# Kernel optimization log

Hardware: AMD Instinct MI355X
Metric: run time of the kernel (lower is better)

## Reference

```python
import jax, jax.numpy as jnp
import numpy as np

B, T, D, H = 512, 128, 256, 512  # batch, seq_len, input_dim, hidden_dim
L = T  # dense output size == seq_len


def setup_inputs() -> dict:
    key = jax.random.key(0)
    ks = jax.random.split(key, 12)
    s = 0.05
    return {
        "inputs": jax.random.normal(ks[0], (B, T, D), jnp.float32),
        "target_indices": jax.random.randint(ks[1], (B, T), 0, T),
        "enc_Wih": jax.random.normal(ks[2], (4 * H, D), jnp.float32) * s,
        "enc_Whh": jax.random.normal(ks[3], (4 * H, H), jnp.float32) * s,
        "enc_bih": jnp.zeros((4 * H,), jnp.float32),
        "enc_bhh": jnp.zeros((4 * H,), jnp.float32),
        "dec_Wih": jax.random.normal(ks[4], (4 * H, D), jnp.float32) * s,
        "dec_Whh": jax.random.normal(ks[5], (4 * H, H), jnp.float32) * s,
        "dec_bih": jnp.zeros((4 * H,), jnp.float32),
        "dec_bhh": jnp.zeros((4 * H,), jnp.float32),
        "Wd": jax.random.normal(ks[6], (L, H), jnp.float32) * s,
        "bd": jnp.zeros((L,), jnp.float32),
        "Wr": jax.random.normal(ks[7], (4, H), jnp.float32) * (2.0 / np.sqrt(H)),
        "br": jnp.zeros((4,), jnp.float32),
    }


def _lstm_cell(x, h, c, Wih, Whh, bih, bhh):
    gates = x @ Wih.T + h @ Whh.T + bih + bhh
    i, f, g, o = jnp.split(gates, 4, axis=-1)  # torch gate order i,f,g,o
    c = jax.nn.sigmoid(f) * c + jax.nn.sigmoid(i) * jnp.tanh(g)
    h = jax.nn.sigmoid(o) * jnp.tanh(c)
    return h, c


def reference(inputs, target_indices, enc_Wih, enc_Whh, enc_bih, enc_bhh,
              dec_Wih, dec_Whh, dec_bih, dec_bhh, Wd, bd, Wr, br):
    b, t, d = inputs.shape
    hdim = enc_Whh.shape[1]

    # Encoder LSTM over time (identical every step in the original -> compute once)
    def enc_step(carry, x_t):
        h, c = carry
        h, c = _lstm_cell(x_t, h, c, enc_Wih, enc_Whh, enc_bih, enc_bhh)
        return (h, c), h

    h0 = jnp.zeros((b, hdim), inputs.dtype)
    _, enc_hs = jax.lax.scan(enc_step, (h0, h0), inputs.transpose(1, 0, 2))
    enc = enc_hs.transpose(1, 0, 2)  # [B, T, H]

    batch_ar = jnp.arange(b)

    def dec_step(carry, idx_t):
        h, c, mask, x = carry
        h, c = _lstm_cell(x, h, c, dec_Wih, dec_Whh, dec_bih, dec_bhh)
        scores = jnp.einsum('bh,bth->bt', h, enc)
        attn = jax.nn.softmax(scores, axis=-1)
        ctx = jnp.einsum('bt,bth->bh', attn, enc)
        logits = ctx @ Wd.T + bd                       # [B, L]
        logits = jnp.where(mask > 0, -jnp.inf, logits)  # mask previously selected
        rot = ctx @ Wr.T + br                          # [B, 4]
        idx = jnp.clip(idx_t, 0, t - 1)
        mask = jnp.maximum(mask, jax.nn.one_hot(idx, mask.shape[1], dtype=mask.dtype))
        x_next = inputs[batch_ar, idx]
        return (h, c, mask, x_next), (logits, rot)

    mask0 = jnp.zeros((b, Wd.shape[0]), inputs.dtype)
    x0 = jnp.zeros((b, d), inputs.dtype)
    _, (all_logits, all_rot) = jax.lax.scan(
        dec_step, (h0, h0, mask0, x0), target_indices.T)
    return all_logits.transpose(1, 0, 2), all_rot.transpose(1, 0, 2)
```

## Files before the change

kernel.cpp:

```cpp
#include <hip/hip_runtime.h>
#include <hip/hip_bf16.h>
#include <hip/hip_fp16.h>
#include <math.h>

#define B_ 512
#define T_ 128
#define D_ 256
#define H_ 512
#define L_ 128

#define NEG_BIG (-1e30f)

typedef __hip_bfloat16 bf16;
typedef _Float16 f16x8 __attribute__((ext_vector_type(8)));
typedef float f32x4 __attribute__((ext_vector_type(4)));

__device__ __forceinline__ f32x4 mfma16(f16x8 a, f16x8 b, f32x4 c) {
  return __builtin_amdgcn_mfma_f32_16x16x32_f16(a, b, c, 0, 0, 0);
}

__device__ __forceinline__ float sigm(float x) { return 1.0f / (1.0f + expf(-x)); }

__device__ __forceinline__ float bf2f_bits(unsigned short u) {
  unsigned int i = ((unsigned int)u) << 16;
  float f; __builtin_memcpy(&f, &i, 4);
  return f;
}
__device__ __forceinline__ unsigned short f2bf_bits(float f) {
  unsigned int i; __builtin_memcpy(&i, &f, 4);
  unsigned int r = i + 0x7FFFu + ((i >> 16) & 1u);
  return (unsigned short)(r >> 16);
}

template <int F32>
__device__ __forceinline__ float ld1t(const void* base, size_t idx) {
  if (F32) return ((const float*)base)[idx];
  unsigned short u; __builtin_memcpy(&u, (const bf16*)base + idx, 2);
  return bf2f_bits(u);
}
template <int F32>
__device__ __forceinline__ void load8t(const void* base, size_t idx, float* d) {
  if (F32) {
    float4 x = *(const float4*)((const float*)base + idx);
    float4 y = *(const float4*)((const float*)base + idx + 4);
    d[0] = x.x; d[1] = x.y; d[2] = x.z; d[3] = x.w;
    d[4] = y.x; d[5] = y.y; d[6] = y.z; d[7] = y.w;
  } else {
    union { float4 f4; unsigned short u[8]; } q;
    q.f4 = *(const float4*)((const bf16*)base + idx);
#pragma unroll
    for (int i = 0; i < 8; ++i) d[i] = bf2f_bits(q.u[i]);
  }
}
template <int F32>
__device__ __forceinline__ void st1t(void* base, size_t idx, float v) {
  if (F32) ((float*)base)[idx] = v;
  else {
    unsigned short u = f2bf_bits(v);
    __builtin_memcpy((bf16*)base + idx, &u, 2);
  }
}

__global__ void probe_kernel(const void* x, int* flag) {
  __shared__ int cnt;
  if (threadIdx.x == 0) cnt = 0;
  __syncthreads();
  const unsigned short* u = (const unsigned short*)x;
  int wild = 0;
  for (int i = threadIdx.x; i < 16384; i += 256) {
    float v = bf2f_bits(u[2 * i]);
    float av = fabsf(v);
    if (!(av <= 1024.0f) || (v != 0.0f && av < 1e-20f)) wild++;
  }
  atomicAdd(&cnt, wild);
  __syncthreads();
  if (threadIdx.x == 0) flag[0] = (cnt > 512) ? 1 : 0;
}

__global__ void zero_kernel(float* __restrict__ p, int n4) {
  int i = blockIdx.x * blockDim.x + threadIdx.x;
  if (i < n4) ((float4*)p)[i] = make_float4(0.f, 0.f, 0.f, 0.f);
}

__global__ void first_sel_kernel(const int* __restrict__ tidx, int* __restrict__ fs) {
  __shared__ int row[L_];
  __shared__ int idxs[T_];
  int b = blockIdx.x;
  row[threadIdx.x] = 1 << 30;
  int v = tidx[b * T_ + threadIdx.x];
  idxs[threadIdx.x] = min(max(v, 0), T_ - 1);
  __syncthreads();
  if (threadIdx.x == 0) {
    for (int s = 0; s < T_; ++s) {
      int idx = idxs[s];
      if (row[idx] > s) row[idx] = s;
    }
  }
  __syncthreads();
  fs[b * L_ + threadIdx.x] = row[threadIdx.x];
}

template <int F32>
__device__ void pack_w_body(const void* Wih, const void* Whh, const void* bih,
                            const void* bhh, __half* Wpk, float* bs) {
  int np = blockIdx.x;
  int g = np & 3, j = np >> 2;
  int worig = g * H_ + j;
  for (int k = threadIdx.x; k < D_ + H_; k += 256) {
    float v = (k < D_) ? ld1t<F32>(Wih, (size_t)worig * D_ + k)
                       : ld1t<F32>(Whh, (size_t)worig * H_ + (k - D_));
    Wpk[(size_t)np * (D_ + H_) + k] = __float2half(v);
  }
  if (threadIdx.x == 0)
    bs[np] = ld1t<F32>(bih, worig) + ld1t<F32>(bhh, worig);
}
__global__ __launch_bounds__(256) void pack_w(const void* Wih, const void* Whh,
    const void* bih, const void* bhh, __half* Wpk, float* bs, const int* flagp) {
  if (*flagp) pack_w_body<1>(Wih, Whh, bih, bhh, Wpk, bs);
  else        pack_w_body<0>(Wih, Whh, bih, bhh, Wpk, bs);
}

template <int F32>
__device__ void pack16_body(const void* src, __half* dst, int n8) {
  int i = blockIdx.x * blockDim.x + threadIdx.x;
  if (i >= n8) return;
  float w[8];
  load8t<F32>(src, (size_t)i * 8, w);
  union { float4 f4; __half h[8]; } u;
#pragma unroll
  for (int q = 0; q < 8; ++q) u.h[q] = __float2half(w[q]);
  *(float4*)(dst + (size_t)i * 8) = u.f4;
}
__global__ __launch_bounds__(256) void pack16(const void* src, __half* dst, int n8,
                                              const int* flagp) {
  if (*flagp) pack16_body<1>(src, dst, n8);
  else        pack16_body<0>(src, dst, n8);
}

__global__ __launch_bounds__(256) void gather_x(const __half* __restrict__ X16,
                                                const int* __restrict__ tidx,
                                                __half* __restrict__ Xdec) {
  const int row = blockIdx.x * 8 + (threadIdx.x >> 5);
  const int c8 = (threadIdx.x & 31) * 8;
  const int b = row >> 7;
  const int s = row & (T_ - 1);
  float4 v;
  if (s == 0) {
    v = make_float4(0.f, 0.f, 0.f, 0.f);
  } else {
    int tsel = min(max(tidx[b * T_ + s - 1], 0), T_ - 1);
    v = *(const float4*)(X16 + ((size_t)b * T_ + tsel) * D_ + c8);
  }
  *(float4*)(Xdec + (size_t)row * D_ + c8) = v;
}

__global__ __launch_bounds__(256) void transpose_enc(const __half* __restrict__ enc,
                                                     __half* __restrict__ encT) {
  __shared__ __half tile[32][33];
  const int b = blockIdx.x;
  const int t0 = blockIdx.y * 32;
  const int h0 = blockIdx.z * 32;
  const int c = threadIdx.x & 31;
  const int r = threadIdx.x >> 5;
#pragma unroll
  for (int rr = 0; rr < 32; rr += 8)
    tile[rr + r][c] = enc[((size_t)b * T_ + t0 + rr + r) * H_ + h0 + c];
  __syncthreads();
#pragma unroll
  for (int rr = 0; rr < 32; rr += 8)
    encT[((size_t)b * H_ + h0 + rr + r) * T_ + t0 + c] = tile[c][rr + r];
}

__device__ __forceinline__ void cell_epi(const f32x4& acc, const float4& bias,
                                         float& c, unsigned short* hdst,
                                         int bb, int t, int jj) {
  float gi = acc[0] + bias.x;
  float gf = acc[1] + bias.y;
  float gg = acc[2] + bias.z;
  float go = acc[3] + bias.w;
  c = sigm(gf) * c + sigm(gi) * tanhf(gg);
  float hh = sigm(go) * tanhf(c);
  unsigned short hu = __half_as_ushort(__float2half(hh));
  __hip_atomic_store(hdst + ((size_t)bb * T_ + t) * H_ + jj, hu,
                     __ATOMIC_RELAXED, __HIP_MEMORY_SCOPE_AGENT);
}

__global__ __launch_bounds__(256, 2) void lstm_persist(
    const __half* __restrict__ Xenc, const __half* __restrict__ Xdec,
    const __half* __restrict__ WpkE, const float* __restrict__ bsE,
    const __half* __restrict__ WpkD, const float* __restrict__ bsD,
    __half* __restrict__ enc, __half* __restrict__ hdec, int* __restrict__ bar) {
  const int tid = threadIdx.x;
  const int lane = tid & 63;
  const int w = tid >> 6;
  const int r15 = lane & 15;
  const int g4 = lane >> 4;
  const int m0 = blockIdx.x * 64 + (w >> 1) * 32;
  const int b0 = blockIdx.y * 64 + (w & 1) * 32;
  const int bb0 = b0 + r15;
  const int bb1 = bb0 + 16;
  const int p = blockIdx.z;
  int* flags = bar + (p * 8 + blockIdx.y) * 64;
  const int fl = lane & 31;
  const f32x4 z4 = {0.f, 0.f, 0.f, 0.f};

  const __half* Wpk = p ? WpkD : WpkE;
  const float* bs = p ? bsD : bsE;
  const __half* Xp = p ? Xdec : Xenc;
  __half* hbuf = p ? hdec : enc;
  unsigned short* hw = (unsigned short*)hbuf;
  const __half* hb = hbuf;
  const __half* aXp0 = Wpk + (size_t)(m0 + r15) * (D_ + H_) + g4 * 8;
  const __half* aXp1 = aXp0 + (size_t)16 * (D_ + H_);
  f16x8 aH0[16], aH1[16];
#pragma unroll
  for (int ks = 0; ks < 16; ++ks) {
    aH0[ks] = *(const f16x8*)(aXp0 + D_ + ks * 32);
    aH1[ks] = *(const f16x8*)(aXp1 + D_ + ks * 32);
  }
  const int nb0 = m0 + g4 * 4;
  const float4 bias0 = *(const float4*)(bs + nb0);
  const float4 bias1 = *(const float4*)(bs + nb0 + 16);
  const int j0 = nb0 >> 2;
  const int j1 = j0 + 4;
  float c00 = 0.f, c01 = 0.f, c10 = 0.f, c11 = 0.f;

  for (int t = 0; t < T_; ++t) {
    f32x4 acc00 = z4, acc01 = z4, acc10 = z4, acc11 = z4;
    {
      const __half* x0p = Xp + ((size_t)bb0 * T_ + t) * D_ + g4 * 8;
      const __half* x1p = Xp + ((size_t)bb1 * T_ + t) * D_ + g4 * 8;
#pragma unroll
      for (int ks = 0; ks < 8; ++ks) {
        f16x8 a0 = *(const f16x8*)(aXp0 + ks * 32);
        f16x8 a1 = *(const f16x8*)(aXp1 + ks * 32);
        f16x8 bx0 = *(const f16x8*)(x0p + ks * 32);
        f16x8 bx1 = *(const f16x8*)(x1p + ks * 32);
        acc00 = mfma16(a0, bx0, acc00);
        acc01 = mfma16(a0, bx1, acc01);
        acc10 = mfma16(a1, bx0, acc10);
        acc11 = mfma16(a1, bx1, acc11);
      }
    }
    if (t) {
      int v = __hip_atomic_load(flags + fl, __ATOMIC_RELAXED,
                                __HIP_MEMORY_SCOPE_AGENT);
      while (!__all(v >= t)) {
        __builtin_amdgcn_s_sleep(1);
        v = __hip_atomic_load(flags + fl, __ATOMIC_RELAXED,
                              __HIP_MEMORY_SCOPE_AGENT);
      }
      const __half* h0p = hb + ((size_t)bb0 * T_ + (t - 1)) * H_ + g4 * 8;
      const __half* h1p = hb + ((size_t)bb1 * T_ + (t - 1)) * H_ + g4 * 8;
      asm volatile("" : "+v"(h0p), "+v"(h1p));
#pragma unroll
      for (int ks = 0; ks < 16; ++ks) {
        f16x8 bh0 = *(const f16x8*)(h0p + ks * 32);
        f16x8 bh1 = *(const f16x8*)(h1p + ks * 32);
        acc00 = mfma16(aH0[ks], bh0, acc00);
        acc01 = mfma16(aH0[ks], bh1, acc01);
        acc10 = mfma16(aH1[ks], bh0, acc10);
        acc11 = mfma16(aH1[ks], bh1, acc11);
      }
    }
    cell_epi(acc00, bias0, c00, hw, bb0, t, j0);
    cell_epi(acc01, bias0, c01, hw, bb1, t, j0);
    cell_epi(acc10, bias1, c10, hw, bb0, t, j1);
    cell_epi(acc11, bias1, c11, hw, bb1, t, j1);
    if (t + 1 < T_) {
      __syncthreads();
      if (tid == 0)
        __hip_atomic_store(flags + blockIdx.x, t + 1, __ATOMIC_RELAXED,
                           __HIP_MEMORY_SCOPE_AGENT);
    }
  }
}

template <int F32>
__device__ void attend_body(const __half* __restrict__ hdec, const __half* __restrict__ enc,
                            const __half* __restrict__ encT, const __half* __restrict__ Wd16,
                            const void* __restrict__ bd, const void* __restrict__ Wr,
                            const void* __restrict__ br, const int* __restrict__ fs,
                            void* __restrict__ out) {
  __shared__ __align__(16) __half Plds[4][16 * 128];
  __shared__ __align__(16) __half Clds[4][16 * 128];
  const int b = blockIdx.x;
  const int sbase = blockIdx.y * 64;
  const int tid = threadIdx.x;
  const int lane = tid & 63;
  const int w = tid >> 6;
  const int r15 = lane & 15;
  const int g4 = lane >> 4;
  const int sw = sbase + w * 16;
  const __half* encb = enc + (size_t)b * T_ * H_;
  const f32x4 z4 = {0.f, 0.f, 0.f, 0.f};
  f32x4 sacc[8];
#pragma unroll
  for (int i = 0; i < 8; ++i) sacc[i] = z4;
  {
    const __half* hdp = hdec + ((size_t)b * T_ + (sw + r15)) * H_ + g4 * 8;
    for (int k0 = 0; k0 < H_; k0 += 32) {
      f16x8 bv = *(const f16x8*)(hdp + k0);
      const __half* ap = encb + (size_t)r15 * H_ + g4 * 8 + k0;
#pragma unroll
      for (int ms = 0; ms < 8; ++ms)
        sacc[ms] = mfma16(*(const f16x8*)(ap + (size_t)ms * 16 * H_), bv, sacc[ms]);
    }
  }
  float mx = -INFINITY;
#pragma unroll
  for (int ms = 0; ms < 8; ++ms)
#pragma unroll
    for (int q = 0; q < 4; ++q) mx = fmaxf(mx, sacc[ms][q]);
  mx = fmaxf(mx, __shfl_xor(mx, 16));
  mx = fmaxf(mx, __shfl_xor(mx, 32));
  float sum = 0.f;
  float pv[32];
#pragma unroll
  for (int ms = 0; ms < 8; ++ms)
#pragma unroll
    for (int q = 0; q < 4; ++q) {
      float e = expf(sacc[ms][q] - mx);
      pv[ms * 4 + q] = e;
      sum += e;
    }
  sum += __shfl_xor(sum, 16);
  sum += __shfl_xor(sum, 32);
  const float inv = 1.0f / sum;
  {
    char* pw = (char*)Plds[w];
    const int swz = (r15 & 7) << 4;
#pragma unroll
    for (int ms = 0; ms < 8; ++ms)
#pragma unroll
      for (int q = 0; q < 4; ++q) {
        int t = ms * 16 + g4 * 4 + q;
        *(__half*)(pw + r15 * 256 + ((t * 2) ^ swz)) = __float2half(pv[ms * 4 + q] * inv);
      }
  }
  __syncthreads();
  f32x4 lacc[8];
#pragma unroll
  for (int i = 0; i < 8; ++i) lacc[i] = z4;
  float racc = 0.f;
  const int sl4 = lane >> 2;
  const int rr4 = lane & 3;
  const char* pr = (const char*)Plds[w];
  char* cw = (char*)Clds[w];
  const char* cr = (const char*)Clds[w];
  const int aswz = (r15 & 7) << 4;
  for (int hc = 0; hc < 4; ++hc) {
    f32x4 cacc[8];
#pragma unroll
    for (int i = 0; i < 8; ++i) cacc[i] = z4;
#pragma unroll
    for (int k0 = 0; k0 < T_; k0 += 32) {
      f16x8 av = *(const f16x8*)(pr + r15 * 256 + (((k0 + g4 * 8) * 2) ^ aswz));
      const __half* bp = encT + ((size_t)b * H_ + hc * 128 + r15) * T_ + g4 * 8 + k0;
#pragma unroll
      for (int ns = 0; ns < 8; ++ns)
        cacc[ns] = mfma16(av, *(const f16x8*)(bp + (size_t)ns * 16 * T_), cacc[ns]);
    }
    __syncthreads();
#pragma unroll
    for (int ns = 0; ns < 8; ++ns)
#pragma unroll
      for (int q = 0; q < 4; ++q) {
        int s = g4 * 4 + q;
        int h2 = (ns * 16 + r15) * 2;
        *(__half*)(cw + s * 256 + (h2 ^ ((s & 7) << 4))) = __float2half(cacc[ns][q]);
      }
    __syncthreads();
#pragma unroll
    for (int kk = 0; kk < 128; kk += 32) {
      f16x8 av = *(const f16x8*)(cr + r15 * 256 + (((kk + g4 * 8) * 2) ^ aswz));
      const __half* wp = Wd16 + (size_t)r15 * H_ + hc * 128 + kk + g4 * 8;
#pragma unroll
      for (int nl = 0; nl < 8; ++nl)
        lacc[nl] = mfma16(av, *(const f16x8*)(wp + (size_t)nl * 16 * H_), lacc[nl]);
    }
    {
      const int rswz = (sl4 & 7) << 4;
#pragma unroll
      for (int g = 0; g < 16; ++g) {
        union { float4 f4; __half h[8]; } u;
        u.f4 = *(const float4*)(cr + sl4 * 256 + ((g * 16) ^ rswz));
#pragma unroll
        for (int q = 0; q < 8; ++q)
          racc += __half2float(u.h[q]) *
                  ld1t<F32>(Wr, (size_t)rr4 * H_ + hc * 128 + g * 8 + q);
      }
    }
  }
#pragma unroll
  for (int nl = 0; nl < 8; ++nl)
#pragma unroll
    for (int q = 0; q < 4; ++q) {
      int sg = sw + g4 * 4 + q;
      int l = nl * 16 + r15;
      float v = lacc[nl][q] + ld1t<F32>(bd, l);
      if (fs[b * L_ + l] < sg) v = NEG_BIG;
      st1t<F32>(out, ((size_t)b * T_ + sg) * L_ + l, v);
    }
  {
    float v = racc + ld1t<F32>(br, rr4);
    st1t<F32>(out, (size_t)B_ * T_ * L_ + ((size_t)b * T_ + (sw + sl4)) * 4 + rr4, v);
  }
}

__global__ __launch_bounds__(256) void attend_mfma(
    const __half* hdec, const __half* enc, const __half* encT, const __half* Wd16,
    const void* bd, const void* Wr, const void* br, const int* fs, void* out,
    const int* flagp) {
  if (*flagp) attend_body<1>(hdec, enc, encT, Wd16, bd, Wr, br, fs, out);
  else        attend_body<0>(hdec, enc, encT, Wd16, bd, Wr, br, fs, out);
}

static inline size_t al256(size_t x) { return (x + 255) & ~(size_t)255; }

extern "C" void kernel_launch(void* const* d_in, const int* in_sizes, int n_in,
                              void* d_out, int out_size, void* d_ws, size_t ws_size,
                              hipStream_t stream) {
  const void* inputs = d_in[0];
  const int* tidx = (const int*)d_in[1];
  const void* eWih = d_in[2];
  const void* eWhh = d_in[3];
  const void* eBih = d_in[4];
  const void* eBhh = d_in[5];
  const void* dWih = d_in[6];
  const void* dWhh = d_in[7];
  const void* dBih = d_in[8];
  const void* dBhh = d_in[9];
  const void* Wd = d_in[10];
  const void* bd = d_in[11];
  const void* Wr = d_in[12];
  const void* br = d_in[13];

  char* pp = (char*)d_ws;
  int* flag = (int*)pp;        pp += 256;
  int* fs = (int*)pp;          pp += al256((size_t)B_ * L_ * 4);
  __half* WpkE = (__half*)pp;  pp += (size_t)4 * H_ * (D_ + H_) * 2;
  __half* WpkD = (__half*)pp;  pp += (size_t)4 * H_ * (D_ + H_) * 2;
  float* bsE = (float*)pp;     pp += (size_t)4 * H_ * 4;
  float* bsD = (float*)pp;     pp += (size_t)4 * H_ * 4;
  __half* Wd16 = (__half*)pp;  pp += (size_t)L_ * H_ * 2;
  __half* X16 = (__half*)pp;   pp += (size_t)B_ * T_ * D_ * 2;
  __half* enc = (__half*)pp;   pp += (size_t)B_ * T_ * H_ * 2;
  __half* encT = (__half*)pp;  pp += (size_t)B_ * H_ * T_ * 2;
  __half* hdec = (__half*)pp;  pp += (size_t)B_ * T_ * H_ * 2;
  int* bar = (int*)pp;         pp += 4096;
  __half* Xdec = encT;

  probe_kernel<<<1, 256, 0, stream>>>(inputs, flag);
  pack_w<<<4 * H_, 256, 0, stream>>>(eWih, eWhh, eBih, eBhh, WpkE, bsE, flag);
  pack_w<<<4 * H_, 256, 0, stream>>>(dWih, dWhh, dBih, dBhh, WpkD, bsD, flag);
  pack16<<<(B_ * T_ * D_ / 8 + 255) / 256, 256, 0, stream>>>(
      inputs, X16, B_ * T_ * D_ / 8, flag);
  pack16<<<(L_ * H_ / 8 + 255) / 256, 256, 0, stream>>>(Wd, Wd16, L_ * H_ / 8, flag);
  first_sel_kernel<<<B_, 128, 0, stream>>>(tidx, fs);
  gather_x<<<B_ * T_ / 8, 256, 0, stream>>>(X16, tidx, Xdec);
  zero_kernel<<<1, 256, 0, stream>>>((float*)bar, 256);

  lstm_persist<<<dim3(32, 8, 2), 256, 0, stream>>>(X16, Xdec, WpkE, bsE, WpkD, bsD,
                                                   enc, hdec, bar);

  transpose_enc<<<dim3(B_, T_ / 32, H_ / 32), 256, 0, stream>>>(enc, encT);

  attend_mfma<<<dim3(B_, 2), 256, 0, stream>>>(hdec, enc, encT, Wd16, bd, Wr, br,
                                               fs, d_out, flag);
}
```

Before: 2.098 ms.

## Place LSTM sync groups on a single XCD and stage h through LDS

Re-maps the persistent LSTM grid so that each group of 16 workgroups sharing a batch slice and its flag barrier is scheduled on one XCD, using the round-robin workgroup-to-XCD assignment. It checks HW_REG_XCC_ID at runtime and uses plain stores when the whole group is co-located, falling back to agent-scope atomics otherwise. Tiles grow to 128 gate rows × 32 batch per workgroup. The hidden state is staged through swizzled LDS so each thread writes one coalesced 8-byte chunk instead of scattered 2-byte atomics. The goal is cheaper cross-workgroup communication and fewer global stores. The cost is an extra __syncthreads, a startup handshake, and a dependence on the dispatch-order assumption.

```diff
diff --git a/kernel.cpp b/kernel.cpp
--- a/kernel.cpp
+++ b/kernel.cpp
@@ -171,45 +171,37 @@
     encT[((size_t)b * H_ + h0 + rr + r) * T_ + t0 + c] = tile[c][rr + r];
 }
 
-__device__ __forceinline__ void cell_epi(const f32x4& acc, const float4& bias,
-                                         float& c, unsigned short* hdst,
-                                         int bb, int t, int jj) {
+#define SWZ(b, j) ((j) ^ (((b) & 7) << 2))
+
+__device__ __forceinline__ void cell_f(const f32x4& acc, const float4& bias,
+                                       float& c, float* hh) {
   float gi = acc[0] + bias.x;
   float gf = acc[1] + bias.y;
   float gg = acc[2] + bias.z;
   float go = acc[3] + bias.w;
   c = sigm(gf) * c + sigm(gi) * tanhf(gg);
-  float hh = sigm(go) * tanhf(c);
-  unsigned short hu = __half_as_ushort(__float2half(hh));
-  __hip_atomic_store(hdst + ((size_t)bb * T_ + t) * H_ + jj, hu,
-                     __ATOMIC_RELAXED, __HIP_MEMORY_SCOPE_AGENT);
-}
-
-__global__ __launch_bounds__(256, 2) void lstm_persist(
-    const __half* __restrict__ Xenc, const __half* __restrict__ Xdec,
-    const __half* __restrict__ WpkE, const float* __restrict__ bsE,
-    const __half* __restrict__ WpkD, const float* __restrict__ bsD,
-    __half* __restrict__ enc, __half* __restrict__ hdec, int* __restrict__ bar) {
+  *hh = sigm(go) * tanhf(c);
+}
+
+template <int FAST>
+__device__ void lstm_chain(const __half* __restrict__ Xp,
+                           const __half* __restrict__ Wpk,
+                           const float* __restrict__ bs,
+                           __half* __restrict__ hbuf,
+                           int tile, int bg, int* __restrict__ flags) {
+  __shared__ __half hstage[32][32];
   const int tid = threadIdx.x;
   const int lane = tid & 63;
   const int w = tid >> 6;
   const int r15 = lane & 15;
   const int g4 = lane >> 4;
-  const int m0 = blockIdx.x * 64 + (w >> 1) * 32;
-  const int b0 = blockIdx.y * 64 + (w & 1) * 32;
+  const int m0 = tile * 128 + w * 32;
+  const int b0 = bg * 32;
   const int bb0 = b0 + r15;
   const int bb1 = bb0 + 16;
-  const int p = blockIdx.z;
-  int* flags = bar + (p * 8 + blockIdx.y) * 64;
-  const int fl = lane & 31;
+  const int fl = lane & 15;
   const f32x4 z4 = {0.f, 0.f, 0.f, 0.f};
 
-  const __half* Wpk = p ? WpkD : WpkE;
-  const float* bs = p ? bsD : bsE;
-  const __half* Xp = p ? Xdec : Xenc;
-  __half* hbuf = p ? hdec : enc;
-  unsigned short* hw = (unsigned short*)hbuf;
-  const __half* hb = hbuf;
   const __half* aXp0 = Wpk + (size_t)(m0 + r15) * (D_ + H_) + g4 * 8;
   const __half* aXp1 = aXp0 + (size_t)16 * (D_ + H_);
   f16x8 aH0[16], aH1[16];
@@ -221,9 +213,14 @@
   const int nb0 = m0 + g4 * 4;
   const float4 bias0 = *(const float4*)(bs + nb0);
   const float4 bias1 = *(const float4*)(bs + nb0 + 16);
-  const int j0 = nb0 >> 2;
-  const int j1 = j0 + 4;
+  const int jrel0 = w * 8 + g4;
+  const int jrel1 = jrel0 + 4;
   float c00 = 0.f, c01 = 0.f, c10 = 0.f, c11 = 0.f;
+  const int srow = tid >> 3;
+  const int schk = tid & 7;
+  const int sposl = SWZ(srow, schk * 4);
+  unsigned long long* gdst = (unsigned long long*)hbuf;
+  const size_t gcol = (size_t)tile * 32 + schk * 4;
 
   for (int t = 0; t < T_; ++t) {
     f32x4 acc00 = z4, acc01 = z4, acc10 = z4, acc11 = z4;
@@ -250,8 +247,8 @@
         v = __hip_atomic_load(flags + fl, __ATOMIC_RELAXED,
                               __HIP_MEMORY_SCOPE_AGENT);
       }
-      const __half* h0p = hb + ((size_t)bb0 * T_ + (t - 1)) * H_ + g4 * 8;
-      const __half* h1p = hb + ((size_t)bb1 * T_ + (t - 1)) * H_ + g4 * 8;
+      const __half* h0p = hbuf + ((size_t)bb0 * T_ + (t - 1)) * H_ + g4 * 8;
+      const __half* h1p = hbuf + ((size_t)bb1 * T_ + (t - 1)) * H_ + g4 * 8;
       asm volatile("" : "+v"(h0p), "+v"(h1p));
 #pragma unroll
       for (int ks = 0; ks < 16; ++ks) {
@@ -263,16 +260,72 @@
         acc11 = mfma16(aH1[ks], bh1, acc11);
       }
     }
-    cell_epi(acc00, bias0, c00, hw, bb0, t, j0);
-    cell_epi(acc01, bias0, c01, hw, bb1, t, j0);
-    cell_epi(acc10, bias1, c10, hw, bb0, t, j1);
-    cell_epi(acc11, bias1, c11, hw, bb1, t, j1);
+    float h00, h01, h10, h11;
+    cell_f(acc00, bias0, c00, &h00);
+    cell_f(acc01, bias0, c01, &h01);
+    cell_f(acc10, bias1, c10, &h10);
+    cell_f(acc11, bias1, c11, &h11);
+    hstage[r15][SWZ(r15, jrel0)] = __float2half(h00);
+    hstage[r15 + 16][SWZ(r15 + 16, jrel0)] = __float2half(h01);
+    hstage[r15][SWZ(r15, jrel1)] = __float2half(h10);
+    hstage[r15 + 16][SWZ(r15 + 16, jrel1)] = __float2half(h11);
+    __syncthreads();
+    {
+      unsigned long long val =
+          *(const unsigned long long*)&hstage[srow][sposl];
+      size_t gi = ((((size_t)(b0 + srow) * T_ + t) * H_) + gcol) >> 2;
+      if (FAST)
+        gdst[gi] = val;
+      else
+        __hip_atomic_store(gdst + gi, val, __ATOMIC_RELAXED,
+                           __HIP_MEMORY_SCOPE_AGENT);
+    }
     if (t + 1 < T_) {
       __syncthreads();
       if (tid == 0)
-        __hip_atomic_store(flags + blockIdx.x, t + 1, __ATOMIC_RELAXED,
+        __hip_atomic_store(flags + tile, t + 1, __ATOMIC_RELAXED,
                            __HIP_MEMORY_SCOPE_AGENT);
     }
+  }
+}
+
+__global__ __launch_bounds__(256, 2) void lstm_persist(
+    const __half* __restrict__ Xenc, const __half* __restrict__ Xdec,
+    const __half* __restrict__ WpkE, const float* __restrict__ bsE,
+    const __half* __restrict__ WpkD, const float* __restrict__ bsD,
+    __half* __restrict__ enc, __half* __restrict__ hdec, int* __restrict__ bar) {
+  const int wgid = blockIdx.x;
+  const int xcd = wgid & 7;
+  const int tile = (wgid >> 3) & 15;
+  const int q = wgid >> 7;
+  const int g = q * 8 + xcd;
+  const int p = g >> 4;
+  const int bg = g & 15;
+  int* flags = bar + g * 16;
+  int* xcca = bar + 512 + g * 16;
+  const int tid = threadIdx.x;
+  const int lane = tid & 63;
+
+  int xcc;
+  asm volatile("s_getreg_b32 %0, hwreg(HW_REG_XCC_ID)" : "=s"(xcc));
+  if (tid == 0)
+    __hip_atomic_store(xcca + tile, xcc + 1, __ATOMIC_RELAXED,
+                       __HIP_MEMORY_SCOPE_AGENT);
+  int vv = __hip_atomic_load(xcca + (lane & 15), __ATOMIC_RELAXED,
+                             __HIP_MEMORY_SCOPE_AGENT);
+  while (!__all(vv != 0)) {
+    __builtin_amdgcn_s_sleep(1);
+    vv = __hip_atomic_load(xcca + (lane & 15), __ATOMIC_RELAXED,
+                           __HIP_MEMORY_SCOPE_AGENT);
+  }
+  const int fast = __all(vv == (xcc + 1));
+
+  if (p == 0) {
+    if (fast) lstm_chain<1>(Xenc, WpkE, bsE, enc, tile, bg, flags);
+    else      lstm_chain<0>(Xenc, WpkE, bsE, enc, tile, bg, flags);
+  } else {
+    if (fast) lstm_chain<1>(Xdec, WpkD, bsD, hdec, tile, bg, flags);
+    else      lstm_chain<0>(Xdec, WpkD, bsD, hdec, tile, bg, flags);
   }
 }
 
@@ -448,7 +501,7 @@
   __half* enc = (__half*)pp;   pp += (size_t)B_ * T_ * H_ * 2;
   __half* encT = (__half*)pp;  pp += (size_t)B_ * H_ * T_ * 2;
   __half* hdec = (__half*)pp;  pp += (size_t)B_ * T_ * H_ * 2;
-  int* bar = (int*)pp;         pp += 4096;
+  int* bar = (int*)pp;         pp += 8192;
   __half* Xdec = encT;
 
   probe_kernel<<<1, 256, 0, stream>>>(inputs, flag);
@@ -459,10 +512,10 @@
   pack16<<<(L_ * H_ / 8 + 255) / 256, 256, 0, stream>>>(Wd, Wd16, L_ * H_ / 8, flag);
   first_sel_kernel<<<B_, 128, 0, stream>>>(tidx, fs);
   gather_x<<<B_ * T_ / 8, 256, 0, stream>>>(X16, tidx, Xdec);
-  zero_kernel<<<1, 256, 0, stream>>>((float*)bar, 256);
-
-  lstm_persist<<<dim3(32, 8, 2), 256, 0, stream>>>(X16, Xdec, WpkE, bsE, WpkD, bsD,
-                                                   enc, hdec, bar);
+  zero_kernel<<<2, 256, 0, stream>>>((float*)bar, 512);
+
+  lstm_persist<<<512, 256, 0, stream>>>(X16, Xdec, WpkE, bsE, WpkD, bsD,
+                                        enc, hdec, bar);
 
   transpose_enc<<<dim3(B_, T_ / 32, H_ / 32), 256, 0, stream>>>(enc, encT);
 
```

New measurement: 2.347 ms. +11.9%, slower.

## Repartition persistent LSTM with LDS-resident swizzled weights and staged coalesced h stores

Applied to the files above, without the earlier changes.

The persistent LSTM kernel now runs as 512 flat workgroups. Each one owns 32 gate rows and 128 batch rows, and loads its packed Wih|Whh slice once into XOR-swizzled LDS instead of keeping the recurrent weights in registers. Hidden outputs are staged in LDS and written as 16-byte coalesced stores, replacing scattered 2-byte atomic stores. The kernel reads the XCC ID so it can use plain stores when all cooperating groups share an XCC, and the sigmoid and tanh use fast __expf forms. The aim is lower register pressure, fewer global weight reads and cheaper h writes per step. The costs are LDS traffic for every weight fragment, reliance on cross-group visibility on the fast path, and flag and XCC slots that may not be fully cleared by the existing zero kernel.

```diff
diff --git a/kernel.cpp b/kernel.cpp
--- a/kernel.cpp
+++ b/kernel.cpp
@@ -19,7 +19,10 @@
   return __builtin_amdgcn_mfma_f32_16x16x32_f16(a, b, c, 0, 0, 0);
 }
 
-__device__ __forceinline__ float sigm(float x) { return 1.0f / (1.0f + expf(-x)); }
+__device__ __forceinline__ float fsigm(float x) { return 1.0f / (1.0f + __expf(-x)); }
+__device__ __forceinline__ float ftanh(float x) {
+  return 1.0f - 2.0f / (__expf(2.0f * x) + 1.0f);
+}
 
 __device__ __forceinline__ float bf2f_bits(unsigned short u) {
   unsigned int i = ((unsigned int)u) << 16;
@@ -171,59 +174,71 @@
     encT[((size_t)b * H_ + h0 + rr + r) * T_ + t0 + c] = tile[c][rr + r];
 }
 
-__device__ __forceinline__ void cell_epi(const f32x4& acc, const float4& bias,
-                                         float& c, unsigned short* hdst,
-                                         int bb, int t, int jj) {
-  float gi = acc[0] + bias.x;
-  float gf = acc[1] + bias.y;
-  float gg = acc[2] + bias.z;
-  float go = acc[3] + bias.w;
-  c = sigm(gf) * c + sigm(gi) * tanhf(gg);
-  float hh = sigm(go) * tanhf(c);
-  unsigned short hu = __half_as_ushort(__float2half(hh));
-  __hip_atomic_store(hdst + ((size_t)bb * T_ + t) * H_ + jj, hu,
-                     __ATOMIC_RELAXED, __HIP_MEMORY_SCOPE_AGENT);
-}
-
 __global__ __launch_bounds__(256, 2) void lstm_persist(
     const __half* __restrict__ Xenc, const __half* __restrict__ Xdec,
     const __half* __restrict__ WpkE, const float* __restrict__ bsE,
     const __half* __restrict__ WpkD, const float* __restrict__ bsD,
     __half* __restrict__ enc, __half* __restrict__ hdec, int* __restrict__ bar) {
+  __shared__ __align__(16) __half Wlds[32 * 768];
+  __shared__ __align__(16) __half hstage[128][8];
   const int tid = threadIdx.x;
   const int lane = tid & 63;
   const int w = tid >> 6;
   const int r15 = lane & 15;
   const int g4 = lane >> 4;
-  const int m0 = blockIdx.x * 64 + (w >> 1) * 32;
-  const int b0 = blockIdx.y * 64 + (w & 1) * 32;
-  const int bb0 = b0 + r15;
-  const int bb1 = bb0 + 16;
-  const int p = blockIdx.z;
-  int* flags = bar + (p * 8 + blockIdx.y) * 64;
-  const int fl = lane & 31;
+  const int wgid = blockIdx.x;
+  const int tile = wgid >> 3;
+  const int g = wgid & 7;
+  const int p = g >> 2;
+  const int bg = g & 3;
+  int* flags = bar + g * 64;
+  int* xcca = bar + 512 + g * 64;
   const f32x4 z4 = {0.f, 0.f, 0.f, 0.f};
 
   const __half* Wpk = p ? WpkD : WpkE;
   const float* bs = p ? bsD : bsE;
   const __half* Xp = p ? Xdec : Xenc;
   __half* hbuf = p ? hdec : enc;
-  unsigned short* hw = (unsigned short*)hbuf;
-  const __half* hb = hbuf;
-  const __half* aXp0 = Wpk + (size_t)(m0 + r15) * (D_ + H_) + g4 * 8;
-  const __half* aXp1 = aXp0 + (size_t)16 * (D_ + H_);
-  f16x8 aH0[16], aH1[16];
-#pragma unroll
-  for (int ks = 0; ks < 16; ++ks) {
-    aH0[ks] = *(const f16x8*)(aXp0 + D_ + ks * 32);
-    aH1[ks] = *(const f16x8*)(aXp1 + D_ + ks * 32);
-  }
-  const int nb0 = m0 + g4 * 4;
+
+  int xcc;
+  asm volatile("s_getreg_b32 %0, hwreg(HW_REG_XCC_ID)" : "=s"(xcc));
+  if (tid == 0)
+    __hip_atomic_store(xcca + tile, xcc + 1, __ATOMIC_RELAXED,
+                       __HIP_MEMORY_SCOPE_AGENT);
+  int vv = __hip_atomic_load(xcca + lane, __ATOMIC_RELAXED,
+                             __HIP_MEMORY_SCOPE_AGENT);
+  while (!__all(vv != 0)) {
+    __builtin_amdgcn_s_sleep(1);
+    vv = __hip_atomic_load(xcca + lane, __ATOMIC_RELAXED,
+                           __HIP_MEMORY_SCOPE_AGENT);
+  }
+  const int fast = __all(vv == (xcc + 1));
+
+  {
+    const char* src = (const char*)(Wpk + (size_t)(tile * 32) * (D_ + H_));
+    char* dst = (char*)Wlds;
+#pragma unroll
+    for (int it = 0; it < 12; ++it) {
+      int c = tid + it * 256;
+      int row = c / 96;
+      int kb = (c % 96) * 16;
+      *(float4*)(dst + row * 1536 + (kb ^ ((row & 7) << 4))) =
+          *(const float4*)(src + c * 16);
+    }
+  }
+  const int nb0 = tile * 32 + g4 * 4;
   const float4 bias0 = *(const float4*)(bs + nb0);
   const float4 bias1 = *(const float4*)(bs + nb0 + 16);
-  const int j0 = nb0 >> 2;
-  const int j1 = j0 + 4;
+  const int b0w = bg * 128 + w * 32;
+  const int bb0 = b0w + r15;
+  const int bb1 = bb0 + 16;
+  const char* Wb = (const char*)Wlds;
+  const int xm = (r15 & 7) << 4;
+  const int rb0 = r15 * 1536;
+  const int rb1 = (r15 + 16) * 1536;
+  const int g16 = g4 * 16;
   float c00 = 0.f, c01 = 0.f, c10 = 0.f, c11 = 0.f;
+  __syncthreads();
 
   for (int t = 0; t < T_; ++t) {
     f32x4 acc00 = z4, acc01 = z4, acc10 = z4, acc11 = z4;
@@ -232,8 +247,8 @@
       const __half* x1p = Xp + ((size_t)bb1 * T_ + t) * D_ + g4 * 8;
 #pragma unroll
       for (int ks = 0; ks < 8; ++ks) {
-        f16x8 a0 = *(const f16x8*)(aXp0 + ks * 32);
-        f16x8 a1 = *(const f16x8*)(aXp1 + ks * 32);
+        f16x8 a0 = *(const f16x8*)(Wb + rb0 + ((ks * 64 + g16) ^ xm));
+        f16x8 a1 = *(const f16x8*)(Wb + rb1 + ((ks * 64 + g16) ^ xm));
         f16x8 bx0 = *(const f16x8*)(x0p + ks * 32);
         f16x8 bx1 = *(const f16x8*)(x1p + ks * 32);
         acc00 = mfma16(a0, bx0, acc00);
@@ -243,34 +258,66 @@
       }
     }
     if (t) {
-      int v = __hip_atomic_load(flags + fl, __ATOMIC_RELAXED,
+      int v = __hip_atomic_load(flags + lane, __ATOMIC_RELAXED,
                                 __HIP_MEMORY_SCOPE_AGENT);
       while (!__all(v >= t)) {
         __builtin_amdgcn_s_sleep(1);
-        v = __hip_atomic_load(flags + fl, __ATOMIC_RELAXED,
+        v = __hip_atomic_load(flags + lane, __ATOMIC_RELAXED,
                               __HIP_MEMORY_SCOPE_AGENT);
       }
-      const __half* h0p = hb + ((size_t)bb0 * T_ + (t - 1)) * H_ + g4 * 8;
-      const __half* h1p = hb + ((size_t)bb1 * T_ + (t - 1)) * H_ + g4 * 8;
+      const __half* h0p = hbuf + ((size_t)bb0 * T_ + (t - 1)) * H_ + g4 * 8;
+      const __half* h1p = hbuf + ((size_t)bb1 * T_ + (t - 1)) * H_ + g4 * 8;
       asm volatile("" : "+v"(h0p), "+v"(h1p));
 #pragma unroll
       for (int ks = 0; ks < 16; ++ks) {
+        f16x8 a0 = *(const f16x8*)(Wb + rb0 + ((512 + ks * 64 + g16) ^ xm));
+        f16x8 a1 = *(const f16x8*)(Wb + rb1 + ((512 + ks * 64 + g16) ^ xm));
         f16x8 bh0 = *(const f16x8*)(h0p + ks * 32);
         f16x8 bh1 = *(const f16x8*)(h1p + ks * 32);
-        acc00 = mfma16(aH0[ks], bh0, acc00);
-        acc01 = mfma16(aH0[ks], bh1, acc01);
-        acc10 = mfma16(aH1[ks], bh0, acc10);
-        acc11 = mfma16(aH1[ks], bh1, acc11);
-      }
-    }
-    cell_epi(acc00, bias0, c00, hw, bb0, t, j0);
-    cell_epi(acc01, bias0, c01, hw, bb1, t, j0);
-    cell_epi(acc10, bias1, c10, hw, bb0, t, j1);
-    cell_epi(acc11, bias1, c11, hw, bb1, t, j1);
+        acc00 = mfma16(a0, bh0, acc00);
+        acc01 = mfma16(a0, bh1, acc01);
+        acc10 = mfma16(a1, bh0, acc10);
+        acc11 = mfma16(a1, bh1, acc11);
+      }
+    }
+    {
+      float gi, gf, gg, go;
+      gi = acc00[0] + bias0.x; gf = acc00[1] + bias0.y;
+      gg = acc00[2] + bias0.z; go = acc00[3] + bias0.w;
+      c00 = fsigm(gf) * c00 + fsigm(gi) * ftanh(gg);
+      hstage[w * 32 + r15][g4] = __float2half(fsigm(go) * ftanh(c00));
+      gi = acc01[0] + bias0.x; gf = acc01[1] + bias0.y;
+      gg = acc01[2] + bias0.z; go = acc01[3] + bias0.w;
+      c01 = fsigm(gf) * c01 + fsigm(gi) * ftanh(gg);
+      hstage[w * 32 + 16 + r15][g4] = __float2half(fsigm(go) * ftanh(c01));
+      gi = acc10[0] + bias1.x; gf = acc10[1] + bias1.y;
+      gg = acc10[2] + bias1.z; go = acc10[3] + bias1.w;
+      c10 = fsigm(gf) * c10 + fsigm(gi) * ftanh(gg);
+      hstage[w * 32 + r15][g4 + 4] = __float2half(fsigm(go) * ftanh(c10));
+      gi = acc11[0] + bias1.x; gf = acc11[1] + bias1.y;
+      gg = acc11[2] + bias1.z; go = acc11[3] + bias1.w;
+      c11 = fsigm(gf) * c11 + fsigm(gi) * ftanh(gg);
+      hstage[w * 32 + 16 + r15][g4 + 4] = __float2half(fsigm(go) * ftanh(c11));
+    }
+    __syncthreads();
+    if (tid < 128) {
+      union { float4 f; unsigned long long u[2]; } val;
+      val.f = *(const float4*)&hstage[tid][0];
+      size_t off = ((size_t)(bg * 128 + tid) * T_ + t) * H_ + tile * 8;
+      if (fast) {
+        *(float4*)(hbuf + off) = val.f;
+      } else {
+        unsigned long long* q = (unsigned long long*)(hbuf + off);
+        __hip_atomic_store(q, val.u[0], __ATOMIC_RELAXED,
+                           __HIP_MEMORY_SCOPE_AGENT);
+        __hip_atomic_store(q + 1, val.u[1], __ATOMIC_RELAXED,
+                           __HIP_MEMORY_SCOPE_AGENT);
+      }
+    }
     if (t + 1 < T_) {
       __syncthreads();
       if (tid == 0)
-        __hip_atomic_store(flags + blockIdx.x, t + 1, __ATOMIC_RELAXED,
+        __hip_atomic_store(flags + tile, t + 1, __ATOMIC_RELAXED,
                            __HIP_MEMORY_SCOPE_AGENT);
     }
   }
@@ -448,7 +495,7 @@
   __half* enc = (__half*)pp;   pp += (size_t)B_ * T_ * H_ * 2;
   __half* encT = (__half*)pp;  pp += (size_t)B_ * H_ * T_ * 2;
   __half* hdec = (__half*)pp;  pp += (size_t)B_ * T_ * H_ * 2;
-  int* bar = (int*)pp;         pp += 4096;
+  int* bar = (int*)pp;         pp += 8192;
   __half* Xdec = encT;
 
   probe_kernel<<<1, 256, 0, stream>>>(inputs, flag);
@@ -461,8 +508,8 @@
   gather_x<<<B_ * T_ / 8, 256, 0, stream>>>(X16, tidx, Xdec);
   zero_kernel<<<1, 256, 0, stream>>>((float*)bar, 256);
 
-  lstm_persist<<<dim3(32, 8, 2), 256, 0, stream>>>(X16, Xdec, WpkE, bsE, WpkD, bsD,
-                                                   enc, hdec, bar);
+  lstm_persist<<<512, 256, 0, stream>>>(X16, Xdec, WpkE, bsE, WpkD, bsD,
+                                        enc, hdec, bar);
 
   transpose_enc<<<dim3(B_, T_ / 32, H_ / 32), 256, 0, stream>>>(enc, encT);
 
```

Measured after the change: 1.971 ms. 1.06x faster.
